# Optimization experiments

Measured on AMD Instinct MI355X. Metric: run time of the kernel, lower is better.

The kernel has to match this reference:

```python
import jax, jax.numpy as jnp
import numpy as np
from jax import lax

LEAKY_ALPHA = 0.3  # Keras LeakyReLU default


def _conv2d_same(psi, w, b):
    # psi: [B,H,W,Cin], w: [kh,kw,Cin,Cout], b: [Cout]
    y = lax.conv_general_dilated(
        psi, w, window_strides=(1, 1), padding='SAME',
        dimension_numbers=('NHWC', 'HWIO', 'NHWC'))
    y = y + b
    return jnp.where(y > 0, y, LEAKY_ALPHA * y)


def setup_inputs() -> dict:
    key = jax.random.key(0)
    ks = jax.random.split(key, 4)
    B, H, W, BANDS, C = 2, 128, 128, 32, 64
    CPSI = 64
    x = jax.random.normal(ks[0], (B, H, W, BANDS, C), dtype=jnp.float32)
    psi = jax.random.normal(ks[1], (B, H, W, CPSI), dtype=jnp.float32)
    fan_in = 3 * 3 * CPSI
    scale = (2.0 / fan_in) ** 0.5  # he-like init for conv weights
    gamma_w = jax.random.normal(ks[2], (3, 3, CPSI, C), dtype=jnp.float32) * scale
    beta_w = jax.random.normal(ks[3], (3, 3, CPSI, C), dtype=jnp.float32) * scale
    gamma_b = jnp.zeros((C,), dtype=jnp.float32)
    beta_b = jnp.zeros((C,), dtype=jnp.float32)
    return {"x": x, "psi": psi, "gamma_w": gamma_w, "gamma_b": gamma_b,
            "beta_w": beta_w, "beta_b": beta_b}


def reference(x, psi, gamma_w, gamma_b, beta_w, beta_b):
    # SFT / FiLM: gamma, beta conditioned on psi, broadcast over the band axis.
    gamma = _conv2d_same(psi, gamma_w, gamma_b)  # [B,H,W,C]
    beta = _conv2d_same(psi, beta_w, beta_b)     # [B,H,W,C]
    # Original loops over bands with slice/concat; equivalent to one broadcast.
    return gamma[:, :, :, None, :] * x + beta[:, :, :, None, :]  # [B,H,W,bands,C]
```

## Files before the change

kernel.cpp:

```cpp
#include <hip/hip_runtime.h>


#define LEAKY 0.3f

constexpr int Bc    = 2;
constexpr int Hc    = 128;
constexpr int Wc    = 128;
constexpr int BANDS = 32;
constexpr int C     = 64;
constexpr int CPSI  = 64;
constexpr int COUT2 = 128;
constexpr int NPIX  = Bc * Hc * Wc;

typedef __attribute__((ext_vector_type(8))) short bf16x8;
typedef __attribute__((ext_vector_type(4))) float f32x4;

__device__ __forceinline__ unsigned short f2bf(float v) {
  unsigned int u = __float_as_uint(v);
  u += 0x7fffu + ((u >> 16) & 1u);
  return (unsigned short)(u >> 16);
}
__device__ __forceinline__ float bf2f(unsigned short h) {
  return __uint_as_float(((unsigned int)h) << 16);
}

__global__ __launch_bounds__(256) void split_w(
    const float* __restrict__ gw, const float* __restrict__ bw,
    unsigned short* __restrict__ wt)
{
  int o = blockIdx.x * 256 + threadIdx.x;
  int tap = o >> 14;
  int kp  = (o >> 7) & 127;
  int n   = o & 127;
  int cin = kp & 63;
  const float* src = (n < C) ? gw : bw;
  float v = src[((size_t)tap * 64 + cin) * 64 + (n & 63)];
  unsigned short hi = f2bf(v);
  unsigned short r  = (kp < 64) ? hi : f2bf(v - bf2f(hi));
  wt[((size_t)tap << 14) + (size_t)n * 128 + kp] = r;
}

constexpr int SMEM_BYTES = 3 * 34 * 136 * 2;

__global__ __launch_bounds__(256, 4) void sft_fused(
    const float* __restrict__ psi,
    const unsigned short* __restrict__ wt,
    const float* __restrict__ gbias, const float* __restrict__ bbias,
    const float* __restrict__ x,
    float* __restrict__ out)
{
  __shared__ __align__(16) char smem[SMEM_BYTES];
  auto As = (unsigned short(*)[34][136])smem;
  auto g  = (float(*)[132])smem;

  const int tid = threadIdx.x;
  const int blk = blockIdx.x;
  const int w0  = (blk & 3) * 32;
  const int h   = (blk >> 2) & 127;
  const int b   = blk >> 9;
  const int pix0 = blk * 32;

  for (int c = tid; c < 3 * 34 * 16; c += 256) {
    int ch  = c & 15;
    int col = (c >> 4) % 34;
    int row = (c >> 4) / 34;
    int hh = h + row - 1;
    int ww = w0 + col - 1;
    float4 v = make_float4(0.f, 0.f, 0.f, 0.f);
    if (hh >= 0 && hh < Hc && ww >= 0 && ww < Wc)
      v = *(const float4*)&psi[(((size_t)b * Hc + hh) * Wc + ww) * CPSI + ch * 4];
    ushort4 hi, lo;
    hi.x = f2bf(v.x); lo.x = f2bf(v.x - bf2f(hi.x));
    hi.y = f2bf(v.y); lo.y = f2bf(v.y - bf2f(hi.y));
    hi.z = f2bf(v.z); lo.z = f2bf(v.z - bf2f(hi.z));
    hi.w = f2bf(v.w); lo.w = f2bf(v.w - bf2f(hi.w));
    *(ushort4*)&As[row][col][ch * 4]      = hi;
    *(ushort4*)&As[row][col][64 + ch * 4] = lo;
  }

  const int lane = tid & 63;
  const int wv   = tid >> 6;
  const int nb   = wv * 32;
  const int lrow = lane & 15;
  const int lk8  = (lane >> 4) * 8;

  f32x4 acc[2][2];
#pragma unroll
  for (int i = 0; i < 2; ++i)
#pragma unroll
    for (int j = 0; j < 2; ++j) acc[i][j] = (f32x4){0.f, 0.f, 0.f, 0.f};

  __syncthreads();

  const unsigned short* wl0 = wt + (size_t)(nb + lrow) * 128 + lk8;
  const unsigned short* wl1 = wt + (size_t)(nb + 16 + lrow) * 128 + lk8;

  for (int tap = 0; tap < 9; ++tap) {
    const int r  = tap / 3;
    const int dc = tap % 3;
    const size_t to = (size_t)tap << 14;

#pragma unroll
    for (int kk = 0; kk < 64; kk += 32) {
      bf16x8 ah0 = *(const bf16x8*)&As[r][lrow + dc][kk + lk8];
      bf16x8 ah1 = *(const bf16x8*)&As[r][16 + lrow + dc][kk + lk8];
      bf16x8 al0 = *(const bf16x8*)&As[r][lrow + dc][64 + kk + lk8];
      bf16x8 al1 = *(const bf16x8*)&As[r][16 + lrow + dc][64 + kk + lk8];
      bf16x8 bh0 = *(const bf16x8*)&wl0[to + kk];
      bf16x8 bh1 = *(const bf16x8*)&wl1[to + kk];
      bf16x8 bl0 = *(const bf16x8*)&wl0[to + 64 + kk];
      bf16x8 bl1 = *(const bf16x8*)&wl1[to + 64 + kk];

      acc[0][0] = __builtin_amdgcn_mfma_f32_16x16x32_bf16(ah0, bh0, acc[0][0], 0, 0, 0);
      acc[0][1] = __builtin_amdgcn_mfma_f32_16x16x32_bf16(ah0, bh1, acc[0][1], 0, 0, 0);
      acc[1][0] = __builtin_amdgcn_mfma_f32_16x16x32_bf16(ah1, bh0, acc[1][0], 0, 0, 0);
      acc[1][1] = __builtin_amdgcn_mfma_f32_16x16x32_bf16(ah1, bh1, acc[1][1], 0, 0, 0);
      acc[0][0] = __builtin_amdgcn_mfma_f32_16x16x32_bf16(al0, bh0, acc[0][0], 0, 0, 0);
      acc[0][1] = __builtin_amdgcn_mfma_f32_16x16x32_bf16(al0, bh1, acc[0][1], 0, 0, 0);
      acc[1][0] = __builtin_amdgcn_mfma_f32_16x16x32_bf16(al1, bh0, acc[1][0], 0, 0, 0);
      acc[1][1] = __builtin_amdgcn_mfma_f32_16x16x32_bf16(al1, bh1, acc[1][1], 0, 0, 0);
      acc[0][0] = __builtin_amdgcn_mfma_f32_16x16x32_bf16(ah0, bl0, acc[0][0], 0, 0, 0);
      acc[0][1] = __builtin_amdgcn_mfma_f32_16x16x32_bf16(ah0, bl1, acc[0][1], 0, 0, 0);
      acc[1][0] = __builtin_amdgcn_mfma_f32_16x16x32_bf16(ah1, bl0, acc[1][0], 0, 0, 0);
      acc[1][1] = __builtin_amdgcn_mfma_f32_16x16x32_bf16(ah1, bl1, acc[1][1], 0, 0, 0);
    }
  }

  __syncthreads();
#pragma unroll
  for (int nf = 0; nf < 2; ++nf) {
    const int n = nb + nf * 16 + lrow;
    const float bias = (n < C) ? gbias[n] : bbias[n - C];
#pragma unroll
    for (int mf = 0; mf < 2; ++mf) {
#pragma unroll
      for (int rr = 0; rr < 4; ++rr) {
        int m = mf * 16 + (lane >> 4) * 4 + rr;
        float v = acc[mf][nf][rr] + bias;
        g[m][n] = v > 0.f ? v : LEAKY * v;
      }
    }
  }
  __syncthreads();

  const int c0 = (tid * 4) & 63;
  const size_t pbase = (size_t)pix0 * 2048 + (size_t)tid * 4;
#pragma unroll 4
  for (int p = 0; p < 32; ++p) {
    f32x4 ga = *(const f32x4*)&g[p][c0];
    f32x4 be = *(const f32x4*)&g[p][64 + c0];
    size_t a = pbase + (size_t)p * 2048;
    f32x4 x0 = __builtin_nontemporal_load((const f32x4*)&x[a]);
    f32x4 x1 = __builtin_nontemporal_load((const f32x4*)&x[a + 1024]);
    f32x4 o0, o1;
#pragma unroll
    for (int e = 0; e < 4; ++e) {
      o0[e] = fmaf(ga[e], x0[e], be[e]);
      o1[e] = fmaf(ga[e], x1[e], be[e]);
    }
    __builtin_nontemporal_store(o0, (f32x4*)&out[a]);
    __builtin_nontemporal_store(o1, (f32x4*)&out[a + 1024]);
  }
}

__global__ __launch_bounds__(256) void film_fused_slow(
    const float* __restrict__ psi,
    const float* __restrict__ gw, const float* __restrict__ gbias,
    const float* __restrict__ bw, const float* __restrict__ bbias,
    const float* __restrict__ x,
    float* __restrict__ out)
{
  const int pix = blockIdx.x;
  const int w = pix % Wc;
  const int h = (pix / Wc) % Hc;
  const int b = pix / (Wc * Hc);
  __shared__ float pshal[9 * CPSI];
  __shared__ float g[COUT2];
  const int t = threadIdx.x;

  if (t < 144) {
    int j = t * 4;
    int k = j % CPSI;
    int tap = j / CPSI;
    int r = tap / 3, s = tap % 3;
    int hh = h + r - 1, ww = w + s - 1;
    float4 v = make_float4(0.f, 0.f, 0.f, 0.f);
    if (hh >= 0 && hh < Hc && ww >= 0 && ww < Wc)
      v = *(const float4*)&psi[(((size_t)b * Hc + hh) * Wc + ww) * CPSI + k];
    *(float4*)&pshal[j] = v;
  }
  __syncthreads();

  if (t < COUT2) {
    int c = t & 63;
    const float* W_ = (t < C) ? gw : bw;
    float acc = (t < C) ? gbias[c] : bbias[c];
#pragma unroll 4
    for (int j = 0; j < 576; ++j) acc = fmaf(pshal[j], W_[(size_t)j * 64 + c], acc);
    g[t] = acc > 0.f ? acc : LEAKY * acc;
  }
  __syncthreads();

  const int coff = (t & 7) * 8;
  const size_t base = (size_t)pix * (BANDS * C) + (size_t)t * 8;
  float4 x0 = *(const float4*)&x[base];
  float4 x1 = *(const float4*)&x[base + 4];
  float4 ga0 = *(const float4*)&g[coff];
  float4 ga1 = *(const float4*)&g[coff + 4];
  float4 be0 = *(const float4*)&g[C + coff];
  float4 be1 = *(const float4*)&g[C + coff + 4];
  float4 o0, o1;
  o0.x = fmaf(ga0.x, x0.x, be0.x);
  o0.y = fmaf(ga0.y, x0.y, be0.y);
  o0.z = fmaf(ga0.z, x0.z, be0.z);
  o0.w = fmaf(ga0.w, x0.w, be0.w);
  o1.x = fmaf(ga1.x, x1.x, be1.x);
  o1.y = fmaf(ga1.y, x1.y, be1.y);
  o1.z = fmaf(ga1.z, x1.z, be1.z);
  o1.w = fmaf(ga1.w, x1.w, be1.w);
  *(float4*)&out[base] = o0;
  *(float4*)&out[base + 4] = o1;
}

extern "C" void kernel_launch(void* const* d_in, const int* in_sizes, int n_in,
                              void* d_out, int out_size, void* d_ws, size_t ws_size,
                              hipStream_t stream) {
  const float* x     = (const float*)d_in[0];
  const float* psi   = (const float*)d_in[1];
  const float* gw    = (const float*)d_in[2];
  const float* gbias = (const float*)d_in[3];
  const float* bw    = (const float*)d_in[4];
  const float* bbias = (const float*)d_in[5];
  float* out = (float*)d_out;

  const size_t wsplit_bytes = (size_t)9 * 128 * 128 * 2;

  if (ws_size >= wsplit_bytes) {
    unsigned short* wtp = (unsigned short*)d_ws;
    split_w<<<9 * 128 * 128 / 256, 256, 0, stream>>>(gw, bw, wtp);
    sft_fused<<<NPIX / 32, 256, 0, stream>>>(psi, wtp, gbias, bbias, x, out);
  } else {
    film_fused_slow<<<NPIX, 256, 0, stream>>>(psi, gw, gbias, bw, bbias, x, out);
  }
}
```

Baseline: 464.7 us.

## Split fused SFT kernel into MFMA conv pass and streaming FiLM pass

Adds a path that computes the gamma/beta convolution with MFMA into a workspace buffer, then runs a separate per-pixel FiLM kernel that streams x and writes out. The intent is to decouple the compute-heavy conv from the bandwidth-bound broadcast so the streaming kernel runs at full occupancy without the conv stalling it. The cost is an extra global round trip for gamma/beta and one more kernel launch, and the path needs a larger workspace.

New measurement: 519.3 us. 11.7% more time.

```diff
diff --git a/kernel.cpp b/kernel.cpp
--- a/kernel.cpp
+++ b/kernel.cpp
@@ -42,16 +42,13 @@
 
 constexpr int SMEM_BYTES = 3 * 34 * 136 * 2;
 
-__global__ __launch_bounds__(256, 4) void sft_fused(
+__global__ __launch_bounds__(256, 4) void conv_gb_mfma(
     const float* __restrict__ psi,
     const unsigned short* __restrict__ wt,
     const float* __restrict__ gbias, const float* __restrict__ bbias,
-    const float* __restrict__ x,
-    float* __restrict__ out)
-{
-  __shared__ __align__(16) char smem[SMEM_BYTES];
-  auto As = (unsigned short(*)[34][136])smem;
-  auto g  = (float(*)[132])smem;
+    float* __restrict__ gbuf)
+{
+  __shared__ __align__(16) unsigned short As[3][34][136];
 
   const int tid = threadIdx.x;
   const int blk = blockIdx.x;
@@ -111,6 +108,137 @@
       bf16x8 bl0 = *(const bf16x8*)&wl0[to + 64 + kk];
       bf16x8 bl1 = *(const bf16x8*)&wl1[to + 64 + kk];
 
+      acc[0][0] = __builtin_amdgcn_mfma_f32_16x16x32_bf16(ah0, bh0, acc[0][0], 0, 0, 0);
+      acc[0][1] = __builtin_amdgcn_mfma_f32_16x16x32_bf16(ah0, bh1, acc[0][1], 0, 0, 0);
+      acc[1][0] = __builtin_amdgcn_mfma_f32_16x16x32_bf16(ah1, bh0, acc[1][0], 0, 0, 0);
+      acc[1][1] = __builtin_amdgcn_mfma_f32_16x16x32_bf16(ah1, bh1, acc[1][1], 0, 0, 0);
+      acc[0][0] = __builtin_amdgcn_mfma_f32_16x16x32_bf16(al0, bh0, acc[0][0], 0, 0, 0);
+      acc[0][1] = __builtin_amdgcn_mfma_f32_16x16x32_bf16(al0, bh1, acc[0][1], 0, 0, 0);
+      acc[1][0] = __builtin_amdgcn_mfma_f32_16x16x32_bf16(al1, bh0, acc[1][0], 0, 0, 0);
+      acc[1][1] = __builtin_amdgcn_mfma_f32_16x16x32_bf16(al1, bh1, acc[1][1], 0, 0, 0);
+      acc[0][0] = __builtin_amdgcn_mfma_f32_16x16x32_bf16(ah0, bl0, acc[0][0], 0, 0, 0);
+      acc[0][1] = __builtin_amdgcn_mfma_f32_16x16x32_bf16(ah0, bl1, acc[0][1], 0, 0, 0);
+      acc[1][0] = __builtin_amdgcn_mfma_f32_16x16x32_bf16(ah1, bl0, acc[1][0], 0, 0, 0);
+      acc[1][1] = __builtin_amdgcn_mfma_f32_16x16x32_bf16(ah1, bl1, acc[1][1], 0, 0, 0);
+    }
+  }
+
+#pragma unroll
+  for (int nf = 0; nf < 2; ++nf) {
+    const int n = nb + nf * 16 + lrow;
+    const float bias = (n < C) ? gbias[n] : bbias[n - C];
+#pragma unroll
+    for (int mf = 0; mf < 2; ++mf) {
+#pragma unroll
+      for (int rr = 0; rr < 4; ++rr) {
+        int m = mf * 16 + (lane >> 4) * 4 + rr;
+        float v = acc[mf][nf][rr] + bias;
+        __builtin_nontemporal_store(v > 0.f ? v : LEAKY * v,
+                                    &gbuf[(size_t)(pix0 + m) * COUT2 + n]);
+      }
+    }
+  }
+}
+
+__global__ __launch_bounds__(256) void film(
+    const float* __restrict__ x,
+    const float* __restrict__ gb,
+    float* __restrict__ out)
+{
+  const int pix = blockIdx.x;
+  __shared__ float g[COUT2];
+  const int t = threadIdx.x;
+  if (t < 32)
+    *(float4*)&g[t * 4] = *(const float4*)&gb[(size_t)pix * COUT2 + t * 4];
+  __syncthreads();
+
+  const int coff = (t & 7) * 8;
+  const size_t base = (size_t)pix * (BANDS * C) + (size_t)t * 8;
+
+  f32x4 x0 = *(const f32x4*)&x[base];
+  f32x4 x1 = *(const f32x4*)&x[base + 4];
+  f32x4 ga0 = *(const f32x4*)&g[coff];
+  f32x4 ga1 = *(const f32x4*)&g[coff + 4];
+  f32x4 be0 = *(const f32x4*)&g[C + coff];
+  f32x4 be1 = *(const f32x4*)&g[C + coff + 4];
+
+  f32x4 o0, o1;
+#pragma unroll
+  for (int e = 0; e < 4; ++e) {
+    o0[e] = fmaf(ga0[e], x0[e], be0[e]);
+    o1[e] = fmaf(ga1[e], x1[e], be1[e]);
+  }
+  __builtin_nontemporal_store(o0, (f32x4*)&out[base]);
+  __builtin_nontemporal_store(o1, (f32x4*)&out[base + 4]);
+}
+
+__global__ __launch_bounds__(256, 4) void sft_fused(
+    const float* __restrict__ psi,
+    const unsigned short* __restrict__ wt,
+    const float* __restrict__ gbias, const float* __restrict__ bbias,
+    const float* __restrict__ x,
+    float* __restrict__ out)
+{
+  __shared__ __align__(16) char smem[SMEM_BYTES];
+  auto As = (unsigned short(*)[34][136])smem;
+  auto g  = (float(*)[132])smem;
+
+  const int tid = threadIdx.x;
+  const int blk = blockIdx.x;
+  const int w0  = (blk & 3) * 32;
+  const int h   = (blk >> 2) & 127;
+  const int b   = blk >> 9;
+  const int pix0 = blk * 32;
+
+  for (int c = tid; c < 3 * 34 * 16; c += 256) {
+    int ch  = c & 15;
+    int col = (c >> 4) % 34;
+    int row = (c >> 4) / 34;
+    int hh = h + row - 1;
+    int ww = w0 + col - 1;
+    float4 v = make_float4(0.f, 0.f, 0.f, 0.f);
+    if (hh >= 0 && hh < Hc && ww >= 0 && ww < Wc)
+      v = *(const float4*)&psi[(((size_t)b * Hc + hh) * Wc + ww) * CPSI + ch * 4];
+    ushort4 hi, lo;
+    hi.x = f2bf(v.x); lo.x = f2bf(v.x - bf2f(hi.x));
+    hi.y = f2bf(v.y); lo.y = f2bf(v.y - bf2f(hi.y));
+    hi.z = f2bf(v.z); lo.z = f2bf(v.z - bf2f(hi.z));
+    hi.w = f2bf(v.w); lo.w = f2bf(v.w - bf2f(hi.w));
+    *(ushort4*)&As[row][col][ch * 4]      = hi;
+    *(ushort4*)&As[row][col][64 + ch * 4] = lo;
+  }
+
+  const int lane = tid & 63;
+  const int wv   = tid >> 6;
+  const int nb   = wv * 32;
+  const int lrow = lane & 15;
+  const int lk8  = (lane >> 4) * 8;
+
+  f32x4 acc[2][2];
+#pragma unroll
+  for (int i = 0; i < 2; ++i)
+#pragma unroll
+    for (int j = 0; j < 2; ++j) acc[i][j] = (f32x4){0.f, 0.f, 0.f, 0.f};
+
+  __syncthreads();
+
+  const unsigned short* wl0 = wt + (size_t)(nb + lrow) * 128 + lk8;
+  const unsigned short* wl1 = wt + (size_t)(nb + 16 + lrow) * 128 + lk8;
+
+  for (int tap = 0; tap < 9; ++tap) {
+    const int r  = tap / 3;
+    const int dc = tap % 3;
+    const size_t to = (size_t)tap << 14;
+#pragma unroll
+    for (int kk = 0; kk < 64; kk += 32) {
+      bf16x8 ah0 = *(const bf16x8*)&As[r][lrow + dc][kk + lk8];
+      bf16x8 ah1 = *(const bf16x8*)&As[r][16 + lrow + dc][kk + lk8];
+      bf16x8 al0 = *(const bf16x8*)&As[r][lrow + dc][64 + kk + lk8];
+      bf16x8 al1 = *(const bf16x8*)&As[r][16 + lrow + dc][64 + kk + lk8];
+      bf16x8 bh0 = *(const bf16x8*)&wl0[to + kk];
+      bf16x8 bh1 = *(const bf16x8*)&wl1[to + kk];
+      bf16x8 bl0 = *(const bf16x8*)&wl0[to + 64 + kk];
+      bf16x8 bl1 = *(const bf16x8*)&wl1[to + 64 + kk];
       acc[0][0] = __builtin_amdgcn_mfma_f32_16x16x32_bf16(ah0, bh0, acc[0][0], 0, 0, 0);
       acc[0][1] = __builtin_amdgcn_mfma_f32_16x16x32_bf16(ah0, bh1, acc[0][1], 0, 0, 0);
       acc[1][0] = __builtin_amdgcn_mfma_f32_16x16x32_bf16(ah1, bh0, acc[1][0], 0, 0, 0);
@@ -234,8 +362,15 @@
   float* out = (float*)d_out;
 
   const size_t wsplit_bytes = (size_t)9 * 128 * 128 * 2;
-
-  if (ws_size >= wsplit_bytes) {
+  const size_t gbuf_bytes   = (size_t)NPIX * COUT2 * 4;
+
+  if (ws_size >= wsplit_bytes + gbuf_bytes) {
+    unsigned short* wtp = (unsigned short*)d_ws;
+    float* gbuf = (float*)((char*)d_ws + wsplit_bytes);
+    split_w<<<9 * 128 * 128 / 256, 256, 0, stream>>>(gw, bw, wtp);
+    conv_gb_mfma<<<NPIX / 32, 256, 0, stream>>>(psi, wtp, gbias, bbias, gbuf);
+    film<<<NPIX, 256, 0, stream>>>(x, gbuf, out);
+  } else if (ws_size >= wsplit_bytes) {
     unsigned short* wtp = (unsigned short*)d_ws;
     split_w<<<9 * 128 * 128 / 256, 256, 0, stream>>>(gw, bw, wtp);
     sft_fused<<<NPIX / 32, 256, 0, stream>>>(psi, wtp, gbias, bbias, x, out);
```
